# Kernel optimization log

Measured on AMD Instinct MI355X. Metric: run time of the kernel, lower is better.

Reference implementation:

```python
import jax, jax.numpy as jnp
import numpy as np

N_NODES = 100000
IN_DIM = 500
HID = 64
N_CLASSES = 47
N_EDGES = 1200000
K_LAYERS = 2


def _spmm_rownorm(edge_index, h, n):
    # Row-normalized D^{-1} A @ h via gather + segment_sum over edge list.
    src, dst = edge_index[0], edge_index[1]
    ones = jnp.ones(src.shape[0], dtype=h.dtype)
    deg = jax.ops.segment_sum(ones, src, num_segments=n)
    inv_deg = 1.0 / jnp.maximum(deg, 1.0)
    msg = h[dst] * inv_deg[src][:, None]  # [E, HID]
    return jax.ops.segment_sum(msg, src, num_segments=n)  # [N, HID]


def setup_inputs() -> dict:
    key = jax.random.key(0)
    ks = jax.random.split(key, 12)
    x = jax.random.normal(ks[0], (N_NODES, IN_DIM), dtype=jnp.float32)
    edge_index_1 = jax.random.randint(ks[1], (2, N_EDGES), 0, N_NODES, dtype=jnp.int32)
    edge_index_2 = jax.random.randint(ks[2], (2, N_EDGES), 0, N_NODES, dtype=jnp.int32)
    s = 0.02
    W_embed = jax.random.normal(ks[3], (IN_DIM, HID), dtype=jnp.float32) * s
    b_embed = jnp.zeros((HID,), dtype=jnp.float32)
    W0 = jax.random.normal(ks[4], (4 * HID, HID), dtype=jnp.float32) * s
    b0 = jnp.zeros((HID,), dtype=jnp.float32)
    W1 = jax.random.normal(ks[5], (4 * HID, HID), dtype=jnp.float32) * s
    b1 = jnp.zeros((HID,), dtype=jnp.float32)
    Wc = jax.random.normal(ks[6], (HID * (K_LAYERS + 1), N_CLASSES), dtype=jnp.float32) * s
    bc = jnp.zeros((N_CLASSES,), dtype=jnp.float32)
    return {"x": x, "edge_index_1": edge_index_1, "edge_index_2": edge_index_2,
            "W_embed": W_embed, "b_embed": b_embed, "W0": W0, "b0": b0,
            "W1": W1, "b1": b1, "Wc": Wc, "bc": bc}


def reference(x, edge_index_1, edge_index_2, W_embed, b_embed, W0, b0, W1, b1, Wc, bc):
    n = x.shape[0]
    r0 = jax.nn.relu(x @ W_embed + b_embed)  # dropout = identity in eval
    reps = [r0]
    r_prev = r0
    for (W, b) in ((W0, b0), (W1, b1)):
        n1 = _spmm_rownorm(edge_index_1, r_prev, n)
        n2 = _spmm_rownorm(edge_index_2, r_prev, n)
        concat = jnp.concatenate([r_prev, n1, r_prev, n2], axis=1)  # ego separation
        r_k = jax.nn.relu(concat @ W + b)
        reps.append(r_k)
        r_prev = r_k
    emb = jnp.concatenate(reps, axis=1)  # [N, HID*(K+1)]
    logits = emb @ Wc + bc
    return logits
```

## Files before the change

kernel.cpp:

```cpp
#include <hip/hip_runtime.h>

namespace {

constexpr int N  = 100000;
constexpr int KD = 500;
constexpr int E  = 1200000;
constexpr int NC = 47;

constexpr int M2  = 2 * N;
constexpr int E2  = 2 * E;
constexpr int NB  = 391;
constexpr int AB  = 586;
constexpr int EBMAX = 8192;

typedef __attribute__((ext_vector_type(8))) short short8;
typedef __attribute__((ext_vector_type(4))) float f32x4;

__device__ __forceinline__ ushort f2bf(float f) {
    union { float f; uint u; } c; c.f = f;
    uint u = c.u + 0x7fffu + ((c.u >> 16) & 1);
    return (ushort)(u >> 16);
}
__device__ __forceinline__ float bflo(uint v) { union { uint u; float f; } c; c.u = v << 16;        return c.f; }
__device__ __forceinline__ float bfhi(uint v) { union { uint u; float f; } c; c.u = v & 0xffff0000u; return c.f; }


__global__ __launch_bounds__(256) void prep_all(const float* __restrict__ We, const float* __restrict__ W0,
                                                const float* __restrict__ W1, const float* __restrict__ Wc,
                                                const float* __restrict__ bc,
                                                int* __restrict__ cursor, ushort* __restrict__ wtE,
                                                ushort* __restrict__ wf0, ushort* __restrict__ wf1,
                                                ushort* __restrict__ wct, float* __restrict__ bcp) {
    int i = blockIdx.x * 256 + threadIdx.x;
    if (i < NB) cursor[i] = i * EBMAX;
    if (i < 64 * 512) {
        int c = i >> 9, k = i & 511;
        wtE[i] = f2bf(k < KD ? We[k * 64 + c] : 0.f);
    }
    if (i < 64 * 192) {
        int c = i / 192, k = i % 192;
        float v0, v1;
        if (k < 64)       { v0 = W0[k * 64 + c] + W0[(128 + k) * 64 + c];
                            v1 = W1[k * 64 + c] + W1[(128 + k) * 64 + c]; }
        else if (k < 128) { v0 = W0[k * 64 + c]; v1 = W1[k * 64 + c]; }
        else              { v0 = W0[(k + 64) * 64 + c]; v1 = W1[(k + 64) * 64 + c]; }
        wf0[i] = f2bf(v0);
        wf1[i] = f2bf(v1);
        wct[i] = f2bf(c < NC ? Wc[k * NC + c] : 0.f);
    }
    if (i < 64) bcp[i] = (i < NC) ? bc[i] : 0.f;
}


__global__ __launch_bounds__(256) void bucket_scatter(const int* __restrict__ src1, const int* __restrict__ dst1,
                                                      const int* __restrict__ src2, const int* __restrict__ dst2,
                                                      int* __restrict__ cursor, uint* __restrict__ ebuf) {
    __shared__ int h[NB];
    __shared__ int claim[NB];
    int t = threadIdx.x;
    int mb[16];
    uint mu[16];
    for (int b = t; b < NB; b += 256) h[b] = 0;
    __syncthreads();
    #pragma unroll
    for (int q = 0; q < 16; ++q) {
        int i = blockIdx.x * 4096 + q * 256 + t;
        if (i < E2) {
            int g = i >= E;
            int idx = i - g * E;
            int s = g ? src2[idx] : src1[idx];
            int d = g ? dst2[idx] : dst1[idx];
            int v = g * N + s;
            mb[q] = v >> 9;
            mu[q] = ((uint)(v & 511) << 17) | (uint)d;
            atomicAdd(&h[mb[q]], 1);
        } else {
            mb[q] = -1;
            mu[q] = 0;
        }
    }
    __syncthreads();
    for (int b = t; b < NB; b += 256)
        claim[b] = h[b] ? atomicAdd(&cursor[b], h[b]) : 0;
    __syncthreads();
    for (int b = t; b < NB; b += 256) h[b] = 0;
    __syncthreads();
    #pragma unroll
    for (int q = 0; q < 16; ++q) {
        if (mb[q] >= 0) {
            int r = atomicAdd(&h[mb[q]], 1);
            ebuf[claim[mb[q]] + r] = mu[q];
        }
    }
}

__global__ __launch_bounds__(256) void csr_finalize(const uint* __restrict__ ebuf, const int* __restrict__ cursor,
                                                    int* __restrict__ rp, int* __restrict__ rpe,
                                                    float* __restrict__ invd, int* __restrict__ col) {
    __shared__ uint eb[EBMAX];
    __shared__ int h[512];
    __shared__ int ex[512];
    __shared__ int ps[256];
    int bid = blockIdx.x;
    int t = threadIdx.x;
    int b0 = bid * EBMAX;
    int cnt = cursor[bid] - b0;
    if (cnt > EBMAX) cnt = EBMAX;
    if (cnt < 0) cnt = 0;
    h[t] = 0; h[t + 256] = 0;
    for (int j = t; j < cnt; j += 256) eb[j] = ebuf[b0 + j];
    __syncthreads();
    for (int j = t; j < cnt; j += 256) atomicAdd(&h[eb[j] >> 17], 1);
    __syncthreads();
    int pv = h[2 * t] + h[2 * t + 1];
    ps[t] = pv;
    __syncthreads();
    for (int off = 1; off < 256; off <<= 1) {
        int x = (t >= off) ? ps[t - off] : 0;
        __syncthreads();
        ps[t] += x;
        __syncthreads();
    }
    int e2 = ps[t] - pv;
    ex[2 * t] = e2;
    ex[2 * t + 1] = e2 + h[2 * t];
    __syncthreads();
    #pragma unroll
    for (int q = 0; q < 2; ++q) {
        int k = q * 256 + t;
        int n = bid * 512 + k;
        if (n < M2) {
            int st = b0 + ex[k];
            int dv = h[k];
            rp[n]  = st;
            rpe[n] = st + dv;
            invd[n] = 1.0f / (float)(dv > 1 ? dv : 1);
        }
    }
    __syncthreads();
    for (int j = t; j < cnt; j += 256) {
        uint u = eb[j];
        int ls = u >> 17;
        int r = atomicAdd(&ex[ls], 1);
        col[b0 + r] = (int)(u & 0x1FFFFu) * 384;
    }
}


__device__ __forceinline__ void stageB(const ushort* __restrict__ Wt, int ldw, int k0, short* Bs) {
    const int tid = threadIdx.x;
    #pragma unroll
    for (int i = 0; i < 2; ++i) {
        int idx = tid + i * 256;
        int c = idx >> 3, qc = (idx & 7) * 8;
        uint4 v = *reinterpret_cast<const uint4*>(Wt + (size_t)c * ldw + k0 + qc);
        *reinterpret_cast<uint4*>(Bs + (((c << 6) + qc) ^ ((c & 7) << 3))) = v;
    }
}

__device__ __forceinline__ void mma64(const short* As, const short* Bs, f32x4 acc[2][4]) {
    const int lane = threadIdx.x & 63;
    const int wrow = (threadIdx.x >> 6) * 32;
    const int llo = lane & 15, lhi = lane >> 4;
    #pragma unroll
    for (int kf = 0; kf < 2; ++kf) {
        const int kb = kf * 32 + lhi * 8;
        short8 a[2], b[4];
        #pragma unroll
        for (int m = 0; m < 2; ++m) {
            int r = wrow + m * 16 + llo;
            a[m] = *reinterpret_cast<const short8*>(As + (((r << 6) + kb) ^ ((r & 7) << 3)));
        }
        #pragma unroll
        for (int n = 0; n < 4; ++n) {
            int c = n * 16 + llo;
            b[n] = *reinterpret_cast<const short8*>(Bs + (((c << 6) + kb) ^ ((c & 7) << 3)));
        }
        #pragma unroll
        for (int m = 0; m < 2; ++m)
            #pragma unroll
            for (int n = 0; n < 4; ++n)
                acc[m][n] = __builtin_amdgcn_mfma_f32_16x16x32_bf16(a[m], b[n], acc[m][n], 0, 0, 0);
    }
}

template<bool OUTF32>
__device__ __forceinline__ void epilogue(f32x4 acc[2][4], const float* __restrict__ bias,
                                         void* out, int ldo, int ocols, int relu, int rbase) {
    const int lane = threadIdx.x & 63;
    const int wrow = (threadIdx.x >> 6) * 32;
    #pragma unroll
    for (int m = 0; m < 2; ++m) {
        #pragma unroll
        for (int r = 0; r < 4; ++r) {
            int orow = rbase + wrow + m * 16 + (lane >> 4) * 4 + r;
            if (orow >= N) continue;
            #pragma unroll
            for (int n = 0; n < 4; ++n) {
                int c = n * 16 + (lane & 15);
                float v = acc[m][n][r] + bias[c];
                if (relu) v = fmaxf(v, 0.f);
                if (OUTF32) {
                    if (c < ocols) ((float*)out)[(size_t)orow * ldo + c] = v;
                } else {
                    ((ushort*)out)[(size_t)orow * ldo + c] = f2bf(v);
                }
            }
        }
    }
}

__global__ __launch_bounds__(256) void gemm_embed(const float* __restrict__ x,
                                                  const ushort* __restrict__ WtE,
                                                  const float* __restrict__ bias,
                                                  ushort* __restrict__ out) {
    __shared__ short As[128 * 64];
    __shared__ short Bs[64 * 64];
    const int tid = threadIdx.x;
    const int rbase = blockIdx.x * 128;
    f32x4 acc[2][4] = {};
    for (int k0 = 0; k0 < 512; k0 += 64) {
        __syncthreads();
        #pragma unroll
        for (int i = 0; i < 8; ++i) {
            int idx = tid + i * 256;
            int r = idx >> 4, qc = (idx & 15) * 4;
            int grow = rbase + r;
            float4 v = {0.f, 0.f, 0.f, 0.f};
            if (grow < N && k0 + qc < KD) v = *reinterpret_cast<const float4*>(x + (size_t)grow * KD + k0 + qc);
            uint2 p;
            p.x = (uint)f2bf(v.x) | ((uint)f2bf(v.y) << 16);
            p.y = (uint)f2bf(v.z) | ((uint)f2bf(v.w) << 16);
            *reinterpret_cast<uint2*>(As + (((r << 6) + qc) ^ ((r & 7) << 3))) = p;
        }
        stageB(WtE, 512, k0, Bs);
        __syncthreads();
        mma64(As, Bs, acc);
    }
    epilogue<false>(acc, bias, out, 192, 64, 1, rbase);
}

template<bool OUTF32>
__global__ __launch_bounds__(256) void gemm3(const ushort* __restrict__ a0, int lda0,
                                             const ushort* __restrict__ a1, int lda1,
                                             const ushort* __restrict__ a2, int lda2,
                                             const ushort* __restrict__ Wt,
                                             const float* __restrict__ bias,
                                             void* out, int ldo, int ocols, int relu) {
    __shared__ short As[128 * 64];
    __shared__ short Bs[64 * 64];
    const int tid = threadIdx.x;
    const int rbase = blockIdx.x * 128;
    f32x4 acc[2][4] = {};
    const ushort* aseg[3] = {a0, a1, a2};
    const int ldas[3] = {lda0, lda1, lda2};
    #pragma unroll
    for (int seg = 0; seg < 3; ++seg) {
        const ushort* A = aseg[seg];
        const int lda = ldas[seg];
        __syncthreads();
        #pragma unroll
        for (int i = 0; i < 4; ++i) {
            int idx = tid + i * 256;
            int r = idx >> 3, qc = (idx & 7) * 8;
            int grow = rbase + r;
            uint4 v = {0u, 0u, 0u, 0u};
            if (grow < N) v = *reinterpret_cast<const uint4*>(A + (size_t)grow * lda + qc);
            *reinterpret_cast<uint4*>(As + (((r << 6) + qc) ^ ((r & 7) << 3))) = v;
        }
        stageB(Wt, 192, seg * 64, Bs);
        __syncthreads();
        mma64(As, Bs, acc);
    }
    epilogue<OUTF32>(acc, bias, out, ldo, ocols, relu, rbase);
}


__global__ __launch_bounds__(256) void spmm7(const int* __restrict__ rp, const int* __restrict__ rpe,
                                             const int* __restrict__ col,
                                             const float* __restrict__ invd,
                                             const ushort* __restrict__ table, int colOff,
                                             ushort* __restrict__ n1b, ushort* __restrict__ n2b) {
    int gid = (blockIdx.x * 256 + threadIdx.x) >> 3;
    int ls = threadIdx.x & 7;
    if (gid >= M2) return;
    const char* hb = (const char*)(table + colOff) + ls * 16;
    float w = invd[gid];
    int s = rp[gid], e = rpe[gid];
    int e1 = e - 1;
    float a0=0.f,a1=0.f,a2=0.f,a3=0.f,a4=0.f,a5=0.f,a6=0.f,a7=0.f;
    for (int j = s; j < e; j += 8) {
        int off[8];
        float wv[8];
        #pragma unroll
        for (int u = 0; u < 8; ++u) {
            int jj = j + u;
            int cidx = jj < e ? jj : e1;
            off[u] = col[cidx];
            wv[u] = jj < e ? 1.f : 0.f;
        }
        uint4 v[8];
        #pragma unroll
        for (int u = 0; u < 8; ++u) v[u] = *reinterpret_cast<const uint4*>(hb + off[u]);
        #pragma unroll
        for (int u = 0; u < 8; ++u) {
            a0 = fmaf(wv[u], bflo(v[u].x), a0); a1 = fmaf(wv[u], bfhi(v[u].x), a1);
            a2 = fmaf(wv[u], bflo(v[u].y), a2); a3 = fmaf(wv[u], bfhi(v[u].y), a3);
            a4 = fmaf(wv[u], bflo(v[u].z), a4); a5 = fmaf(wv[u], bfhi(v[u].z), a5);
            a6 = fmaf(wv[u], bflo(v[u].w), a6); a7 = fmaf(wv[u], bfhi(v[u].w), a7);
        }
    }
    int g = gid >= N;
    int node = gid - g * N;
    ushort* op = g ? n2b : n1b;
    uint4 o;
    o.x = (uint)f2bf(a0 * w) | ((uint)f2bf(a1 * w) << 16);
    o.y = (uint)f2bf(a2 * w) | ((uint)f2bf(a3 * w) << 16);
    o.z = (uint)f2bf(a4 * w) | ((uint)f2bf(a5 * w) << 16);
    o.w = (uint)f2bf(a6 * w) | ((uint)f2bf(a7 * w) << 16);
    *reinterpret_cast<uint4*>(op + (size_t)node * 64 + ls * 8) = o;
}

}

extern "C" void kernel_launch(void* const* d_in, const int* in_sizes, int n_in,
                              void* d_out, int out_size, void* d_ws, size_t ws_size,
                              hipStream_t stream) {
    const float* x       = (const float*)d_in[0];
    const int*   ei1     = (const int*)d_in[1];
    const int*   ei2     = (const int*)d_in[2];
    const float* W_embed = (const float*)d_in[3];
    const float* b_embed = (const float*)d_in[4];
    const float* W0      = (const float*)d_in[5];
    const float* b0      = (const float*)d_in[6];
    const float* W1      = (const float*)d_in[7];
    const float* b1      = (const float*)d_in[8];
    const float* Wc      = (const float*)d_in[9];
    const float* bc      = (const float*)d_in[10];
    float* out = (float*)d_out;

    char* ws = (char*)d_ws;
    size_t off = 0;
    auto alloc = [&](size_t bytes) -> void* {
        void* p = ws + off;
        off += (bytes + 255) & ~(size_t)255;
        return p;
    };

    ushort* embB  = (ushort*)alloc((size_t)N * 192 * 2);
    ushort* n1b   = (ushort*)alloc((size_t)N * 64 * 2);
    ushort* n2b   = (ushort*)alloc((size_t)N * 64 * 2);
    int*    col   = (int*)alloc((size_t)NB * EBMAX * 4);
    uint*   ebuf  = (uint*)alloc((size_t)NB * EBMAX * 4);
    int*    rp    = (int*)alloc((size_t)M2 * 4);
    int*    rpe   = (int*)alloc((size_t)M2 * 4);
    float*  invd  = (float*)alloc((size_t)M2 * 4);
    int*    bcur  = (int*)alloc((NB + 1) * 4);
    ushort* wtE   = (ushort*)alloc(64 * 512 * 2);
    ushort* weff0 = (ushort*)alloc(64 * 192 * 2);
    ushort* weff1 = (ushort*)alloc(64 * 192 * 2);
    ushort* wct   = (ushort*)alloc(64 * 192 * 2);
    float*  bcp   = (float*)alloc(64 * 4);
    if (off > ws_size) return;

    const int* src1 = ei1, *dst1 = ei1 + E;
    const int* src2 = ei2, *dst2 = ei2 + E;

    const int GB = (N + 127) / 128;
    const int PB = (M2 * 8 + 255) / 256;

    prep_all<<<128, 256, 0, stream>>>(W_embed, W0, W1, Wc, bc, bcur, wtE, weff0, weff1, wct, bcp);

    bucket_scatter<<<AB, 256, 0, stream>>>(src1, dst1, src2, dst2, bcur, ebuf);
    csr_finalize<<<NB, 256, 0, stream>>>(ebuf, bcur, rp, rpe, invd, col);

    gemm_embed<<<GB, 256, 0, stream>>>(x, wtE, b_embed, embB);

    for (int layer = 0; layer < 2; ++layer) {
        const ushort* rprev = embB + 64 * layer;
        spmm7<<<PB, 256, 0, stream>>>(rp, rpe, col, invd, embB, 64 * layer, n1b, n2b);
        const ushort* Wl = (layer == 0) ? weff0 : weff1;
        const float*  bl = (layer == 0) ? b0 : b1;
        gemm3<false><<<GB, 256, 0, stream>>>(rprev, 192, n1b, 64, n2b, 64, Wl, bl,
                                             embB + 64 * (layer + 1), 192, 64, 1);
    }

    gemm3<true><<<GB, 256, 0, stream>>>(embB, 192, embB + 64, 192, embB + 128, 192, wct, bcp,
                                        out, NC, NC, 0);
}
```

Measured before the change: 231.0 us.

## Merge CSR finalize with embed GEMM and degree-sort SpMM node schedule

The CSR finalize and the embedding GEMM become one launch that shares memory through a union, so the two independent stages can run at the same time on different CUs. The finalize blocks also counting-sort the nodes of each 512-node bucket by degree and write a permutation. spmm7 walks that permutation so the 8-lane groups in a wavefront handle nodes of similar degree, which cuts divergence from uneven loop trip counts. The costs are an extra indirection load per node, scattered output writes, and the larger shared-memory footprint of the merged kernel, which may lower occupancy for the GEMM blocks.

```diff
diff --git a/kernel.cpp b/kernel.cpp
--- a/kernel.cpp
+++ b/kernel.cpp
@@ -10,6 +10,7 @@
 constexpr int M2  = 2 * N;
 constexpr int E2  = 2 * E;
 constexpr int NB  = 391;
+constexpr int MP  = NB * 512;
 constexpr int AB  = 586;
 constexpr int EBMAX = 8192;
 
@@ -94,58 +95,6 @@
     }
 }
 
-__global__ __launch_bounds__(256) void csr_finalize(const uint* __restrict__ ebuf, const int* __restrict__ cursor,
-                                                    int* __restrict__ rp, int* __restrict__ rpe,
-                                                    float* __restrict__ invd, int* __restrict__ col) {
-    __shared__ uint eb[EBMAX];
-    __shared__ int h[512];
-    __shared__ int ex[512];
-    __shared__ int ps[256];
-    int bid = blockIdx.x;
-    int t = threadIdx.x;
-    int b0 = bid * EBMAX;
-    int cnt = cursor[bid] - b0;
-    if (cnt > EBMAX) cnt = EBMAX;
-    if (cnt < 0) cnt = 0;
-    h[t] = 0; h[t + 256] = 0;
-    for (int j = t; j < cnt; j += 256) eb[j] = ebuf[b0 + j];
-    __syncthreads();
-    for (int j = t; j < cnt; j += 256) atomicAdd(&h[eb[j] >> 17], 1);
-    __syncthreads();
-    int pv = h[2 * t] + h[2 * t + 1];
-    ps[t] = pv;
-    __syncthreads();
-    for (int off = 1; off < 256; off <<= 1) {
-        int x = (t >= off) ? ps[t - off] : 0;
-        __syncthreads();
-        ps[t] += x;
-        __syncthreads();
-    }
-    int e2 = ps[t] - pv;
-    ex[2 * t] = e2;
-    ex[2 * t + 1] = e2 + h[2 * t];
-    __syncthreads();
-    #pragma unroll
-    for (int q = 0; q < 2; ++q) {
-        int k = q * 256 + t;
-        int n = bid * 512 + k;
-        if (n < M2) {
-            int st = b0 + ex[k];
-            int dv = h[k];
-            rp[n]  = st;
-            rpe[n] = st + dv;
-            invd[n] = 1.0f / (float)(dv > 1 ? dv : 1);
-        }
-    }
-    __syncthreads();
-    for (int j = t; j < cnt; j += 256) {
-        uint u = eb[j];
-        int ls = u >> 17;
-        int r = atomicAdd(&ex[ls], 1);
-        col[b0 + r] = (int)(u & 0x1FFFFu) * 384;
-    }
-}
-
 
 __device__ __forceinline__ void stageB(const ushort* __restrict__ Wt, int ldw, int k0, short* Bs) {
     const int tid = threadIdx.x;
@@ -210,34 +159,118 @@
     }
 }
 
-__global__ __launch_bounds__(256) void gemm_embed(const float* __restrict__ x,
-                                                  const ushort* __restrict__ WtE,
-                                                  const float* __restrict__ bias,
-                                                  ushort* __restrict__ out) {
-    __shared__ short As[128 * 64];
-    __shared__ short Bs[64 * 64];
-    const int tid = threadIdx.x;
-    const int rbase = blockIdx.x * 128;
-    f32x4 acc[2][4] = {};
-    for (int k0 = 0; k0 < 512; k0 += 64) {
-        __syncthreads();
-        #pragma unroll
-        for (int i = 0; i < 8; ++i) {
-            int idx = tid + i * 256;
-            int r = idx >> 4, qc = (idx & 15) * 4;
-            int grow = rbase + r;
-            float4 v = {0.f, 0.f, 0.f, 0.f};
-            if (grow < N && k0 + qc < KD) v = *reinterpret_cast<const float4*>(x + (size_t)grow * KD + k0 + qc);
-            uint2 p;
-            p.x = (uint)f2bf(v.x) | ((uint)f2bf(v.y) << 16);
-            p.y = (uint)f2bf(v.z) | ((uint)f2bf(v.w) << 16);
-            *reinterpret_cast<uint2*>(As + (((r << 6) + qc) ^ ((r & 7) << 3))) = p;
-        }
-        stageB(WtE, 512, k0, Bs);
-        __syncthreads();
-        mma64(As, Bs, acc);
-    }
-    epilogue<false>(acc, bias, out, 192, 64, 1, rbase);
+
+union SMem {
+    struct { uint eb[EBMAX]; int h[512]; int ex[512]; int ps[256]; } f;
+    struct { short As[128 * 64]; short Bs[64 * 64]; } g;
+};
+
+__global__ __launch_bounds__(256) void embed_finalize(
+        const float* __restrict__ x, const ushort* __restrict__ WtE,
+        const float* __restrict__ bias, ushort* __restrict__ out,
+        const uint* __restrict__ ebuf, const int* __restrict__ cursor,
+        int* __restrict__ rp, int* __restrict__ rpe, float* __restrict__ invd,
+        int* __restrict__ col, int* __restrict__ nodePerm) {
+    __shared__ SMem sm;
+    const int t = threadIdx.x;
+    if (blockIdx.x < NB) {
+        int bid = blockIdx.x;
+        int b0 = bid * EBMAX;
+        int cnt = cursor[bid] - b0;
+        if (cnt > EBMAX) cnt = EBMAX;
+        if (cnt < 0) cnt = 0;
+        sm.f.h[t] = 0; sm.f.h[t + 256] = 0;
+        for (int j = t; j < cnt; j += 256) sm.f.eb[j] = ebuf[b0 + j];
+        __syncthreads();
+        for (int j = t; j < cnt; j += 256) atomicAdd(&sm.f.h[sm.f.eb[j] >> 17], 1);
+        __syncthreads();
+        int pv = sm.f.h[2 * t] + sm.f.h[2 * t + 1];
+        sm.f.ps[t] = pv;
+        __syncthreads();
+        for (int off = 1; off < 256; off <<= 1) {
+            int xv = (t >= off) ? sm.f.ps[t - off] : 0;
+            __syncthreads();
+            sm.f.ps[t] += xv;
+            __syncthreads();
+        }
+        int e2 = sm.f.ps[t] - pv;
+        sm.f.ex[2 * t] = e2;
+        sm.f.ex[2 * t + 1] = e2 + sm.f.h[2 * t];
+        __syncthreads();
+        #pragma unroll
+        for (int q = 0; q < 2; ++q) {
+            int k = q * 256 + t;
+            int n = bid * 512 + k;
+            if (n < M2) {
+                int st = b0 + sm.f.ex[k];
+                int dv = sm.f.h[k];
+                rp[n]  = st;
+                rpe[n] = st + dv;
+                invd[n] = 1.0f / (float)(dv > 1 ? dv : 1);
+            }
+        }
+        __syncthreads();
+        for (int j = t; j < cnt; j += 256) {
+            uint u = sm.f.eb[j];
+            int ls = u >> 17;
+            int r = atomicAdd(&sm.f.ex[ls], 1);
+            col[b0 + r] = (int)(u & 0x1FFFFu) * 384;
+        }
+        __syncthreads();
+        int* dh  = (int*)sm.f.eb;
+        int* dex = ((int*)sm.f.eb) + 512;
+        dh[t] = 0; dh[t + 256] = 0;
+        __syncthreads();
+        #pragma unroll
+        for (int q = 0; q < 2; ++q) {
+            int k = q * 256 + t;
+            int d = sm.f.h[k]; if (d > 511) d = 511;
+            atomicAdd(&dh[d], 1);
+        }
+        __syncthreads();
+        int pv2 = dh[2 * t] + dh[2 * t + 1];
+        sm.f.ps[t] = pv2;
+        __syncthreads();
+        for (int off = 1; off < 256; off <<= 1) {
+            int xv = (t >= off) ? sm.f.ps[t - off] : 0;
+            __syncthreads();
+            sm.f.ps[t] += xv;
+            __syncthreads();
+        }
+        int e3 = sm.f.ps[t] - pv2;
+        dex[2 * t] = e3;
+        dex[2 * t + 1] = e3 + dh[2 * t];
+        __syncthreads();
+        #pragma unroll
+        for (int q = 0; q < 2; ++q) {
+            int k = q * 256 + t;
+            int d = sm.f.h[k]; if (d > 511) d = 511;
+            int pos = atomicAdd(&dex[d], 1);
+            nodePerm[bid * 512 + pos] = bid * 512 + k;
+        }
+    } else {
+        const int rbase = (blockIdx.x - NB) * 128;
+        f32x4 acc[2][4] = {};
+        for (int k0 = 0; k0 < 512; k0 += 64) {
+            __syncthreads();
+            #pragma unroll
+            for (int i = 0; i < 8; ++i) {
+                int idx = t + i * 256;
+                int r = idx >> 4, qc = (idx & 15) * 4;
+                int grow = rbase + r;
+                float4 v = {0.f, 0.f, 0.f, 0.f};
+                if (grow < N && k0 + qc < KD) v = *reinterpret_cast<const float4*>(x + (size_t)grow * KD + k0 + qc);
+                uint2 p;
+                p.x = (uint)f2bf(v.x) | ((uint)f2bf(v.y) << 16);
+                p.y = (uint)f2bf(v.z) | ((uint)f2bf(v.w) << 16);
+                *reinterpret_cast<uint2*>(sm.g.As + (((r << 6) + qc) ^ ((r & 7) << 3))) = p;
+            }
+            stageB(WtE, 512, k0, sm.g.Bs);
+            __syncthreads();
+            mma64(sm.g.As, sm.g.Bs, acc);
+        }
+        epilogue<false>(acc, bias, out, 192, 64, 1, rbase);
+    }
 }
 
 template<bool OUTF32>
@@ -279,14 +312,17 @@
 __global__ __launch_bounds__(256) void spmm7(const int* __restrict__ rp, const int* __restrict__ rpe,
                                              const int* __restrict__ col,
                                              const float* __restrict__ invd,
+                                             const int* __restrict__ nodePerm,
                                              const ushort* __restrict__ table, int colOff,
                                              ushort* __restrict__ n1b, ushort* __restrict__ n2b) {
-    int gid = (blockIdx.x * 256 + threadIdx.x) >> 3;
+    int sched = (blockIdx.x * 256 + threadIdx.x) >> 3;
     int ls = threadIdx.x & 7;
-    if (gid >= M2) return;
+    if (sched >= MP) return;
+    int node = nodePerm[sched];
+    if (node >= M2) return;
     const char* hb = (const char*)(table + colOff) + ls * 16;
-    float w = invd[gid];
-    int s = rp[gid], e = rpe[gid];
+    float w = invd[node];
+    int s = rp[node], e = rpe[node];
     int e1 = e - 1;
     float a0=0.f,a1=0.f,a2=0.f,a3=0.f,a4=0.f,a5=0.f,a6=0.f,a7=0.f;
     for (int j = s; j < e; j += 8) {
@@ -310,15 +346,15 @@
             a6 = fmaf(wv[u], bflo(v[u].w), a6); a7 = fmaf(wv[u], bfhi(v[u].w), a7);
         }
     }
-    int g = gid >= N;
-    int node = gid - g * N;
+    int g = node >= N;
+    int onode = node - g * N;
     ushort* op = g ? n2b : n1b;
     uint4 o;
     o.x = (uint)f2bf(a0 * w) | ((uint)f2bf(a1 * w) << 16);
     o.y = (uint)f2bf(a2 * w) | ((uint)f2bf(a3 * w) << 16);
     o.z = (uint)f2bf(a4 * w) | ((uint)f2bf(a5 * w) << 16);
     o.w = (uint)f2bf(a6 * w) | ((uint)f2bf(a7 * w) << 16);
-    *reinterpret_cast<uint4*>(op + (size_t)node * 64 + ls * 8) = o;
+    *reinterpret_cast<uint4*>(op + (size_t)onode * 64 + ls * 8) = o;
 }
 
 }
@@ -355,6 +391,7 @@
     int*    rp    = (int*)alloc((size_t)M2 * 4);
     int*    rpe   = (int*)alloc((size_t)M2 * 4);
     float*  invd  = (float*)alloc((size_t)M2 * 4);
+    int*    nperm = (int*)alloc((size_t)MP * 4);
     int*    bcur  = (int*)alloc((NB + 1) * 4);
     ushort* wtE   = (ushort*)alloc(64 * 512 * 2);
     ushort* weff0 = (ushort*)alloc(64 * 192 * 2);
@@ -367,18 +404,18 @@
     const int* src2 = ei2, *dst2 = ei2 + E;
 
     const int GB = (N + 127) / 128;
-    const int PB = (M2 * 8 + 255) / 256;
+    const int PB = (MP * 8 + 255) / 256;
 
     prep_all<<<128, 256, 0, stream>>>(W_embed, W0, W1, Wc, bc, bcur, wtE, weff0, weff1, wct, bcp);
 
     bucket_scatter<<<AB, 256, 0, stream>>>(src1, dst1, src2, dst2, bcur, ebuf);
-    csr_finalize<<<NB, 256, 0, stream>>>(ebuf, bcur, rp, rpe, invd, col);
-
-    gemm_embed<<<GB, 256, 0, stream>>>(x, wtE, b_embed, embB);
+
+    embed_finalize<<<NB + GB, 256, 0, stream>>>(x, wtE, b_embed, embB,
+                                                ebuf, bcur, rp, rpe, invd, col, nperm);
 
     for (int layer = 0; layer < 2; ++layer) {
         const ushort* rprev = embB + 64 * layer;
-        spmm7<<<PB, 256, 0, stream>>>(rp, rpe, col, invd, embB, 64 * layer, n1b, n2b);
+        spmm7<<<PB, 256, 0, stream>>>(rp, rpe, col, invd, nperm, embB, 64 * layer, n1b, n2b);
         const ushort* Wl = (layer == 0) ? weff0 : weff1;
         const float*  bl = (layer == 0) ? b0 : b1;
         gemm3<false><<<GB, 256, 0, stream>>>(rprev, 192, n1b, 64, n2b, 64, Wl, bl,
```

After: 255.1 us. 1.1x slower.

## Schedule SpMM rows sorted by degree within each bucket to reduce wave divergence

Applied to the files above, without the earlier changes.

csr_finalize now runs a second counting sort that orders the 512 rows of each bucket by degree and writes a node permutation. spmm7 reads that permutation, so the 8 row-groups in a wavefront have similar edge counts and the loop trip count varies less across lanes. The cost is an extra indirection load per row group, more work in csr_finalize, and output writes that are no longer contiguous. Nodes in the padding range (beyond 2N) exit early.

```diff
diff --git a/kernel.cpp b/kernel.cpp
--- a/kernel.cpp
+++ b/kernel.cpp
@@ -10,6 +10,7 @@
 constexpr int M2  = 2 * N;
 constexpr int E2  = 2 * E;
 constexpr int NB  = 391;
+constexpr int MP  = NB * 512;
 constexpr int AB  = 586;
 constexpr int EBMAX = 8192;
 
@@ -96,7 +97,8 @@
 
 __global__ __launch_bounds__(256) void csr_finalize(const uint* __restrict__ ebuf, const int* __restrict__ cursor,
                                                     int* __restrict__ rp, int* __restrict__ rpe,
-                                                    float* __restrict__ invd, int* __restrict__ col) {
+                                                    float* __restrict__ invd, int* __restrict__ col,
+                                                    int* __restrict__ nodePerm) {
     __shared__ uint eb[EBMAX];
     __shared__ int h[512];
     __shared__ int ex[512];
@@ -116,9 +118,9 @@
     ps[t] = pv;
     __syncthreads();
     for (int off = 1; off < 256; off <<= 1) {
-        int x = (t >= off) ? ps[t - off] : 0;
-        __syncthreads();
-        ps[t] += x;
+        int xv = (t >= off) ? ps[t - off] : 0;
+        __syncthreads();
+        ps[t] += xv;
         __syncthreads();
     }
     int e2 = ps[t] - pv;
@@ -143,6 +145,38 @@
         int ls = u >> 17;
         int r = atomicAdd(&ex[ls], 1);
         col[b0 + r] = (int)(u & 0x1FFFFu) * 384;
+    }
+    __syncthreads();
+    int* dh  = (int*)eb;
+    int* dex = ((int*)eb) + 512;
+    dh[t] = 0; dh[t + 256] = 0;
+    __syncthreads();
+    #pragma unroll
+    for (int q = 0; q < 2; ++q) {
+        int k = q * 256 + t;
+        int d = h[k]; if (d > 511) d = 511;
+        atomicAdd(&dh[d], 1);
+    }
+    __syncthreads();
+    int pv2 = dh[2 * t] + dh[2 * t + 1];
+    ps[t] = pv2;
+    __syncthreads();
+    for (int off = 1; off < 256; off <<= 1) {
+        int xv = (t >= off) ? ps[t - off] : 0;
+        __syncthreads();
+        ps[t] += xv;
+        __syncthreads();
+    }
+    int e3 = ps[t] - pv2;
+    dex[2 * t] = e3;
+    dex[2 * t + 1] = e3 + dh[2 * t];
+    __syncthreads();
+    #pragma unroll
+    for (int q = 0; q < 2; ++q) {
+        int k = q * 256 + t;
+        int d = h[k]; if (d > 511) d = 511;
+        int pos = atomicAdd(&dex[d], 1);
+        nodePerm[bid * 512 + pos] = bid * 512 + k;
     }
 }
 
@@ -279,14 +313,17 @@
 __global__ __launch_bounds__(256) void spmm7(const int* __restrict__ rp, const int* __restrict__ rpe,
                                              const int* __restrict__ col,
                                              const float* __restrict__ invd,
+                                             const int* __restrict__ nodePerm,
                                              const ushort* __restrict__ table, int colOff,
                                              ushort* __restrict__ n1b, ushort* __restrict__ n2b) {
-    int gid = (blockIdx.x * 256 + threadIdx.x) >> 3;
+    int sched = (blockIdx.x * 256 + threadIdx.x) >> 3;
     int ls = threadIdx.x & 7;
-    if (gid >= M2) return;
+    if (sched >= MP) return;
+    int node = nodePerm[sched];
+    if (node >= M2) return;
     const char* hb = (const char*)(table + colOff) + ls * 16;
-    float w = invd[gid];
-    int s = rp[gid], e = rpe[gid];
+    float w = invd[node];
+    int s = rp[node], e = rpe[node];
     int e1 = e - 1;
     float a0=0.f,a1=0.f,a2=0.f,a3=0.f,a4=0.f,a5=0.f,a6=0.f,a7=0.f;
     for (int j = s; j < e; j += 8) {
@@ -310,15 +347,15 @@
             a6 = fmaf(wv[u], bflo(v[u].w), a6); a7 = fmaf(wv[u], bfhi(v[u].w), a7);
         }
     }
-    int g = gid >= N;
-    int node = gid - g * N;
+    int g = node >= N;
+    int onode = node - g * N;
     ushort* op = g ? n2b : n1b;
     uint4 o;
     o.x = (uint)f2bf(a0 * w) | ((uint)f2bf(a1 * w) << 16);
     o.y = (uint)f2bf(a2 * w) | ((uint)f2bf(a3 * w) << 16);
     o.z = (uint)f2bf(a4 * w) | ((uint)f2bf(a5 * w) << 16);
     o.w = (uint)f2bf(a6 * w) | ((uint)f2bf(a7 * w) << 16);
-    *reinterpret_cast<uint4*>(op + (size_t)node * 64 + ls * 8) = o;
+    *reinterpret_cast<uint4*>(op + (size_t)onode * 64 + ls * 8) = o;
 }
 
 }
@@ -355,6 +392,7 @@
     int*    rp    = (int*)alloc((size_t)M2 * 4);
     int*    rpe   = (int*)alloc((size_t)M2 * 4);
     float*  invd  = (float*)alloc((size_t)M2 * 4);
+    int*    nperm = (int*)alloc((size_t)MP * 4);
     int*    bcur  = (int*)alloc((NB + 1) * 4);
     ushort* wtE   = (ushort*)alloc(64 * 512 * 2);
     ushort* weff0 = (ushort*)alloc(64 * 192 * 2);
@@ -367,18 +405,18 @@
     const int* src2 = ei2, *dst2 = ei2 + E;
 
     const int GB = (N + 127) / 128;
-    const int PB = (M2 * 8 + 255) / 256;
+    const int PB = (MP * 8 + 255) / 256;
 
     prep_all<<<128, 256, 0, stream>>>(W_embed, W0, W1, Wc, bc, bcur, wtE, weff0, weff1, wct, bcp);
 
     bucket_scatter<<<AB, 256, 0, stream>>>(src1, dst1, src2, dst2, bcur, ebuf);
-    csr_finalize<<<NB, 256, 0, stream>>>(ebuf, bcur, rp, rpe, invd, col);
+    csr_finalize<<<NB, 256, 0, stream>>>(ebuf, bcur, rp, rpe, invd, col, nperm);
 
     gemm_embed<<<GB, 256, 0, stream>>>(x, wtE, b_embed, embB);
 
     for (int layer = 0; layer < 2; ++layer) {
         const ushort* rprev = embB + 64 * layer;
-        spmm7<<<PB, 256, 0, stream>>>(rp, rpe, col, invd, embB, 64 * layer, n1b, n2b);
+        spmm7<<<PB, 256, 0, stream>>>(rp, rpe, col, invd, nperm, embB, 64 * layer, n1b, n2b);
         const ushort* Wl = (layer == 0) ? weff0 : weff1;
         const float*  bl = (layer == 0) ? b0 : b1;
         gemm3<false><<<GB, 256, 0, stream>>>(rprev, 192, n1b, 64, n2b, 64, Wl, bl,
```

New measurement: 256.5 us. 1.11x slower.

## Fuse SpMM aggregation into layer GEMM and merge edge scatter with embed GEMM

Applied to the files above, without the earlier changes.

The sparse neighbor aggregation is now computed inside the per-layer GEMM kernel, written straight into the shared-memory A tile instead of round-tripping n1/n2 through global memory. The edge bucket scatter and the embedding GEMM run in one launch with disjoint block ranges, so the two independent jobs can overlap and a launch is dropped. The trade-off is that the gather runs with only GB blocks of 256 threads, each doing 4 rows per thread-group serially, which may reduce memory-level parallelism compared with the standalone SpMM grid.

```diff
diff --git a/kernel.cpp b/kernel.cpp
--- a/kernel.cpp
+++ b/kernel.cpp
@@ -52,45 +52,140 @@
 }
 
 
-__global__ __launch_bounds__(256) void bucket_scatter(const int* __restrict__ src1, const int* __restrict__ dst1,
-                                                      const int* __restrict__ src2, const int* __restrict__ dst2,
-                                                      int* __restrict__ cursor, uint* __restrict__ ebuf) {
-    __shared__ int h[NB];
-    __shared__ int claim[NB];
-    int t = threadIdx.x;
-    int mb[16];
-    uint mu[16];
-    for (int b = t; b < NB; b += 256) h[b] = 0;
-    __syncthreads();
-    #pragma unroll
-    for (int q = 0; q < 16; ++q) {
-        int i = blockIdx.x * 4096 + q * 256 + t;
-        if (i < E2) {
-            int g = i >= E;
-            int idx = i - g * E;
-            int s = g ? src2[idx] : src1[idx];
-            int d = g ? dst2[idx] : dst1[idx];
-            int v = g * N + s;
-            mb[q] = v >> 9;
-            mu[q] = ((uint)(v & 511) << 17) | (uint)d;
-            atomicAdd(&h[mb[q]], 1);
-        } else {
-            mb[q] = -1;
-            mu[q] = 0;
-        }
-    }
-    __syncthreads();
-    for (int b = t; b < NB; b += 256)
-        claim[b] = h[b] ? atomicAdd(&cursor[b], h[b]) : 0;
-    __syncthreads();
-    for (int b = t; b < NB; b += 256) h[b] = 0;
-    __syncthreads();
-    #pragma unroll
-    for (int q = 0; q < 16; ++q) {
-        if (mb[q] >= 0) {
-            int r = atomicAdd(&h[mb[q]], 1);
-            ebuf[claim[mb[q]] + r] = mu[q];
-        }
+__device__ __forceinline__ void stageB(const ushort* __restrict__ Wt, int ldw, int k0, short* Bs) {
+    const int tid = threadIdx.x;
+    #pragma unroll
+    for (int i = 0; i < 2; ++i) {
+        int idx = tid + i * 256;
+        int c = idx >> 3, qc = (idx & 7) * 8;
+        uint4 v = *reinterpret_cast<const uint4*>(Wt + (size_t)c * ldw + k0 + qc);
+        *reinterpret_cast<uint4*>(Bs + (((c << 6) + qc) ^ ((c & 7) << 3))) = v;
+    }
+}
+
+__device__ __forceinline__ void mma64(const short* As, const short* Bs, f32x4 acc[2][4]) {
+    const int lane = threadIdx.x & 63;
+    const int wrow = (threadIdx.x >> 6) * 32;
+    const int llo = lane & 15, lhi = lane >> 4;
+    #pragma unroll
+    for (int kf = 0; kf < 2; ++kf) {
+        const int kb = kf * 32 + lhi * 8;
+        short8 a[2], b[4];
+        #pragma unroll
+        for (int m = 0; m < 2; ++m) {
+            int r = wrow + m * 16 + llo;
+            a[m] = *reinterpret_cast<const short8*>(As + (((r << 6) + kb) ^ ((r & 7) << 3)));
+        }
+        #pragma unroll
+        for (int n = 0; n < 4; ++n) {
+            int c = n * 16 + llo;
+            b[n] = *reinterpret_cast<const short8*>(Bs + (((c << 6) + kb) ^ ((c & 7) << 3)));
+        }
+        #pragma unroll
+        for (int m = 0; m < 2; ++m)
+            #pragma unroll
+            for (int n = 0; n < 4; ++n)
+                acc[m][n] = __builtin_amdgcn_mfma_f32_16x16x32_bf16(a[m], b[n], acc[m][n], 0, 0, 0);
+    }
+}
+
+template<bool OUTF32>
+__device__ __forceinline__ void epilogue(f32x4 acc[2][4], const float* __restrict__ bias,
+                                         void* out, int ldo, int ocols, int relu, int rbase) {
+    const int lane = threadIdx.x & 63;
+    const int wrow = (threadIdx.x >> 6) * 32;
+    #pragma unroll
+    for (int m = 0; m < 2; ++m) {
+        #pragma unroll
+        for (int r = 0; r < 4; ++r) {
+            int orow = rbase + wrow + m * 16 + (lane >> 4) * 4 + r;
+            if (orow >= N) continue;
+            #pragma unroll
+            for (int n = 0; n < 4; ++n) {
+                int c = n * 16 + (lane & 15);
+                float v = acc[m][n][r] + bias[c];
+                if (relu) v = fmaxf(v, 0.f);
+                if (OUTF32) {
+                    if (c < ocols) ((float*)out)[(size_t)orow * ldo + c] = v;
+                } else {
+                    ((ushort*)out)[(size_t)orow * ldo + c] = f2bf(v);
+                }
+            }
+        }
+    }
+}
+
+
+union SMem2 {
+    struct { int h[NB]; int claim[NB]; } s;
+    struct { short As[128 * 64]; short Bs[64 * 64]; } g;
+};
+
+__global__ __launch_bounds__(256) void scatter_embed(
+        const int* __restrict__ src1, const int* __restrict__ dst1,
+        const int* __restrict__ src2, const int* __restrict__ dst2,
+        int* __restrict__ cursor, uint* __restrict__ ebuf,
+        const float* __restrict__ x, const ushort* __restrict__ WtE,
+        const float* __restrict__ bias, ushort* __restrict__ out) {
+    __shared__ SMem2 sm;
+    const int t = threadIdx.x;
+    if (blockIdx.x < AB) {
+        int mb[16];
+        uint mu[16];
+        for (int b = t; b < NB; b += 256) sm.s.h[b] = 0;
+        __syncthreads();
+        #pragma unroll
+        for (int q = 0; q < 16; ++q) {
+            int i = blockIdx.x * 4096 + q * 256 + t;
+            if (i < E2) {
+                int g = i >= E;
+                int idx = i - g * E;
+                int s = g ? src2[idx] : src1[idx];
+                int d = g ? dst2[idx] : dst1[idx];
+                int v = g * N + s;
+                mb[q] = v >> 9;
+                mu[q] = ((uint)(v & 511) << 17) | (uint)d;
+                atomicAdd(&sm.s.h[mb[q]], 1);
+            } else {
+                mb[q] = -1;
+                mu[q] = 0;
+            }
+        }
+        __syncthreads();
+        for (int b = t; b < NB; b += 256)
+            sm.s.claim[b] = sm.s.h[b] ? atomicAdd(&cursor[b], sm.s.h[b]) : 0;
+        __syncthreads();
+        for (int b = t; b < NB; b += 256) sm.s.h[b] = 0;
+        __syncthreads();
+        #pragma unroll
+        for (int q = 0; q < 16; ++q) {
+            if (mb[q] >= 0) {
+                int r = atomicAdd(&sm.s.h[mb[q]], 1);
+                ebuf[sm.s.claim[mb[q]] + r] = mu[q];
+            }
+        }
+    } else {
+        const int rbase = (blockIdx.x - AB) * 128;
+        f32x4 acc[2][4] = {};
+        for (int k0 = 0; k0 < 512; k0 += 64) {
+            __syncthreads();
+            #pragma unroll
+            for (int i = 0; i < 8; ++i) {
+                int idx = t + i * 256;
+                int r = idx >> 4, qc = (idx & 15) * 4;
+                int grow = rbase + r;
+                float4 v = {0.f, 0.f, 0.f, 0.f};
+                if (grow < N && k0 + qc < KD) v = *reinterpret_cast<const float4*>(x + (size_t)grow * KD + k0 + qc);
+                uint2 p;
+                p.x = (uint)f2bf(v.x) | ((uint)f2bf(v.y) << 16);
+                p.y = (uint)f2bf(v.z) | ((uint)f2bf(v.w) << 16);
+                *reinterpret_cast<uint2*>(sm.g.As + (((r << 6) + qc) ^ ((r & 7) << 3))) = p;
+            }
+            stageB(WtE, 512, k0, sm.g.Bs);
+            __syncthreads();
+            mma64(sm.g.As, sm.g.Bs, acc);
+        }
+        epilogue<false>(acc, bias, out, 192, 64, 1, rbase);
     }
 }
 
@@ -116,9 +211,9 @@
     ps[t] = pv;
     __syncthreads();
     for (int off = 1; off < 256; off <<= 1) {
-        int x = (t >= off) ? ps[t - off] : 0;
-        __syncthreads();
-        ps[t] += x;
+        int xv = (t >= off) ? ps[t - off] : 0;
+        __syncthreads();
+        ps[t] += xv;
         __syncthreads();
     }
     int e2 = ps[t] - pv;
@@ -147,71 +242,11 @@
 }
 
 
-__device__ __forceinline__ void stageB(const ushort* __restrict__ Wt, int ldw, int k0, short* Bs) {
-    const int tid = threadIdx.x;
-    #pragma unroll
-    for (int i = 0; i < 2; ++i) {
-        int idx = tid + i * 256;
-        int c = idx >> 3, qc = (idx & 7) * 8;
-        uint4 v = *reinterpret_cast<const uint4*>(Wt + (size_t)c * ldw + k0 + qc);
-        *reinterpret_cast<uint4*>(Bs + (((c << 6) + qc) ^ ((c & 7) << 3))) = v;
-    }
-}
-
-__device__ __forceinline__ void mma64(const short* As, const short* Bs, f32x4 acc[2][4]) {
-    const int lane = threadIdx.x & 63;
-    const int wrow = (threadIdx.x >> 6) * 32;
-    const int llo = lane & 15, lhi = lane >> 4;
-    #pragma unroll
-    for (int kf = 0; kf < 2; ++kf) {
-        const int kb = kf * 32 + lhi * 8;
-        short8 a[2], b[4];
-        #pragma unroll
-        for (int m = 0; m < 2; ++m) {
-            int r = wrow + m * 16 + llo;
-            a[m] = *reinterpret_cast<const short8*>(As + (((r << 6) + kb) ^ ((r & 7) << 3)));
-        }
-        #pragma unroll
-        for (int n = 0; n < 4; ++n) {
-            int c = n * 16 + llo;
-            b[n] = *reinterpret_cast<const short8*>(Bs + (((c << 6) + kb) ^ ((c & 7) << 3)));
-        }
-        #pragma unroll
-        for (int m = 0; m < 2; ++m)
-            #pragma unroll
-            for (int n = 0; n < 4; ++n)
-                acc[m][n] = __builtin_amdgcn_mfma_f32_16x16x32_bf16(a[m], b[n], acc[m][n], 0, 0, 0);
-    }
-}
-
-template<bool OUTF32>
-__device__ __forceinline__ void epilogue(f32x4 acc[2][4], const float* __restrict__ bias,
-                                         void* out, int ldo, int ocols, int relu, int rbase) {
-    const int lane = threadIdx.x & 63;
-    const int wrow = (threadIdx.x >> 6) * 32;
-    #pragma unroll
-    for (int m = 0; m < 2; ++m) {
-        #pragma unroll
-        for (int r = 0; r < 4; ++r) {
-            int orow = rbase + wrow + m * 16 + (lane >> 4) * 4 + r;
-            if (orow >= N) continue;
-            #pragma unroll
-            for (int n = 0; n < 4; ++n) {
-                int c = n * 16 + (lane & 15);
-                float v = acc[m][n][r] + bias[c];
-                if (relu) v = fmaxf(v, 0.f);
-                if (OUTF32) {
-                    if (c < ocols) ((float*)out)[(size_t)orow * ldo + c] = v;
-                } else {
-                    ((ushort*)out)[(size_t)orow * ldo + c] = f2bf(v);
-                }
-            }
-        }
-    }
-}
-
-__global__ __launch_bounds__(256) void gemm_embed(const float* __restrict__ x,
-                                                  const ushort* __restrict__ WtE,
+__global__ __launch_bounds__(256) void gemm_layer(const ushort* __restrict__ rprev,
+                                                  const ushort* __restrict__ table, int colOff,
+                                                  const int* __restrict__ rp, const int* __restrict__ rpe,
+                                                  const int* __restrict__ col, const float* __restrict__ invd,
+                                                  const ushort* __restrict__ Wt,
                                                   const float* __restrict__ bias,
                                                   ushort* __restrict__ out) {
     __shared__ short As[128 * 64];
@@ -219,45 +254,88 @@
     const int tid = threadIdx.x;
     const int rbase = blockIdx.x * 128;
     f32x4 acc[2][4] = {};
-    for (int k0 = 0; k0 < 512; k0 += 64) {
-        __syncthreads();
-        #pragma unroll
-        for (int i = 0; i < 8; ++i) {
-            int idx = tid + i * 256;
-            int r = idx >> 4, qc = (idx & 15) * 4;
+
+    #pragma unroll
+    for (int i = 0; i < 4; ++i) {
+        int idx = tid + i * 256;
+        int r = idx >> 3, qc = (idx & 7) * 8;
+        int grow = rbase + r;
+        uint4 v = {0u, 0u, 0u, 0u};
+        if (grow < N) v = *reinterpret_cast<const uint4*>(rprev + (size_t)grow * 192 + qc);
+        *reinterpret_cast<uint4*>(As + (((r << 6) + qc) ^ ((r & 7) << 3))) = v;
+    }
+    stageB(Wt, 192, 0, Bs);
+    __syncthreads();
+    mma64(As, Bs, acc);
+
+    const int row = tid >> 3;
+    const int ls  = tid & 7;
+    const char* hb = (const char*)(table + colOff) + ls * 16;
+    #pragma unroll
+    for (int g = 0; g < 2; ++g) {
+        __syncthreads();
+        #pragma unroll
+        for (int sw = 0; sw < 4; ++sw) {
+            int r = sw * 32 + row;
             int grow = rbase + r;
-            float4 v = {0.f, 0.f, 0.f, 0.f};
-            if (grow < N && k0 + qc < KD) v = *reinterpret_cast<const float4*>(x + (size_t)grow * KD + k0 + qc);
-            uint2 p;
-            p.x = (uint)f2bf(v.x) | ((uint)f2bf(v.y) << 16);
-            p.y = (uint)f2bf(v.z) | ((uint)f2bf(v.w) << 16);
-            *reinterpret_cast<uint2*>(As + (((r << 6) + qc) ^ ((r & 7) << 3))) = p;
-        }
-        stageB(WtE, 512, k0, Bs);
+            uint4 o = {0u, 0u, 0u, 0u};
+            if (grow < N) {
+                int node = grow + g * N;
+                float w = invd[node];
+                int s = rp[node], e = rpe[node];
+                int e1 = e - 1;
+                float a0=0.f,a1=0.f,a2=0.f,a3=0.f,a4=0.f,a5=0.f,a6=0.f,a7=0.f;
+                for (int j = s; j < e; j += 8) {
+                    int off[8];
+                    float wv[8];
+                    #pragma unroll
+                    for (int u = 0; u < 8; ++u) {
+                        int jj = j + u;
+                        int cidx = jj < e ? jj : e1;
+                        off[u] = col[cidx];
+                        wv[u] = jj < e ? 1.f : 0.f;
+                    }
+                    uint4 v[8];
+                    #pragma unroll
+                    for (int u = 0; u < 8; ++u) v[u] = *reinterpret_cast<const uint4*>(hb + off[u]);
+                    #pragma unroll
+                    for (int u = 0; u < 8; ++u) {
+                        a0 = fmaf(wv[u], bflo(v[u].x), a0); a1 = fmaf(wv[u], bfhi(v[u].x), a1);
+                        a2 = fmaf(wv[u], bflo(v[u].y), a2); a3 = fmaf(wv[u], bfhi(v[u].y), a3);
+                        a4 = fmaf(wv[u], bflo(v[u].z), a4); a5 = fmaf(wv[u], bfhi(v[u].z), a5);
+                        a6 = fmaf(wv[u], bflo(v[u].w), a6); a7 = fmaf(wv[u], bfhi(v[u].w), a7);
+                    }
+                }
+                o.x = (uint)f2bf(a0 * w) | ((uint)f2bf(a1 * w) << 16);
+                o.y = (uint)f2bf(a2 * w) | ((uint)f2bf(a3 * w) << 16);
+                o.z = (uint)f2bf(a4 * w) | ((uint)f2bf(a5 * w) << 16);
+                o.w = (uint)f2bf(a6 * w) | ((uint)f2bf(a7 * w) << 16);
+            }
+            *reinterpret_cast<uint4*>(As + (((r << 6) + ls * 8) ^ ((r & 7) << 3))) = o;
+        }
+        stageB(Wt, 192, (1 + g) * 64, Bs);
         __syncthreads();
         mma64(As, Bs, acc);
     }
     epilogue<false>(acc, bias, out, 192, 64, 1, rbase);
 }
 
-template<bool OUTF32>
-__global__ __launch_bounds__(256) void gemm3(const ushort* __restrict__ a0, int lda0,
-                                             const ushort* __restrict__ a1, int lda1,
-                                             const ushort* __restrict__ a2, int lda2,
-                                             const ushort* __restrict__ Wt,
-                                             const float* __restrict__ bias,
-                                             void* out, int ldo, int ocols, int relu) {
+
+__global__ __launch_bounds__(256) void gemm_cls(const ushort* __restrict__ a0,
+                                                const ushort* __restrict__ a1,
+                                                const ushort* __restrict__ a2,
+                                                const ushort* __restrict__ Wt,
+                                                const float* __restrict__ bias,
+                                                float* __restrict__ out) {
     __shared__ short As[128 * 64];
     __shared__ short Bs[64 * 64];
     const int tid = threadIdx.x;
     const int rbase = blockIdx.x * 128;
     f32x4 acc[2][4] = {};
     const ushort* aseg[3] = {a0, a1, a2};
-    const int ldas[3] = {lda0, lda1, lda2};
     #pragma unroll
     for (int seg = 0; seg < 3; ++seg) {
         const ushort* A = aseg[seg];
-        const int lda = ldas[seg];
         __syncthreads();
         #pragma unroll
         for (int i = 0; i < 4; ++i) {
@@ -265,60 +343,14 @@
             int r = idx >> 3, qc = (idx & 7) * 8;
             int grow = rbase + r;
             uint4 v = {0u, 0u, 0u, 0u};
-            if (grow < N) v = *reinterpret_cast<const uint4*>(A + (size_t)grow * lda + qc);
+            if (grow < N) v = *reinterpret_cast<const uint4*>(A + (size_t)grow * 192 + qc);
             *reinterpret_cast<uint4*>(As + (((r << 6) + qc) ^ ((r & 7) << 3))) = v;
         }
         stageB(Wt, 192, seg * 64, Bs);
         __syncthreads();
         mma64(As, Bs, acc);
     }
-    epilogue<OUTF32>(acc, bias, out, ldo, ocols, relu, rbase);
-}
-
-
-__global__ __launch_bounds__(256) void spmm7(const int* __restrict__ rp, const int* __restrict__ rpe,
-                                             const int* __restrict__ col,
-                                             const float* __restrict__ invd,
-                                             const ushort* __restrict__ table, int colOff,
-                                             ushort* __restrict__ n1b, ushort* __restrict__ n2b) {
-    int gid = (blockIdx.x * 256 + threadIdx.x) >> 3;
-    int ls = threadIdx.x & 7;
-    if (gid >= M2) return;
-    const char* hb = (const char*)(table + colOff) + ls * 16;
-    float w = invd[gid];
-    int s = rp[gid], e = rpe[gid];
-    int e1 = e - 1;
-    float a0=0.f,a1=0.f,a2=0.f,a3=0.f,a4=0.f,a5=0.f,a6=0.f,a7=0.f;
-    for (int j = s; j < e; j += 8) {
-        int off[8];
-        float wv[8];
-        #pragma unroll
-        for (int u = 0; u < 8; ++u) {
-            int jj = j + u;
-            int cidx = jj < e ? jj : e1;
-            off[u] = col[cidx];
-            wv[u] = jj < e ? 1.f : 0.f;
-        }
-        uint4 v[8];
-        #pragma unroll
-        for (int u = 0; u < 8; ++u) v[u] = *reinterpret_cast<const uint4*>(hb + off[u]);
-        #pragma unroll
-        for (int u = 0; u < 8; ++u) {
-            a0 = fmaf(wv[u], bflo(v[u].x), a0); a1 = fmaf(wv[u], bfhi(v[u].x), a1);
-            a2 = fmaf(wv[u], bflo(v[u].y), a2); a3 = fmaf(wv[u], bfhi(v[u].y), a3);
-            a4 = fmaf(wv[u], bflo(v[u].z), a4); a5 = fmaf(wv[u], bfhi(v[u].z), a5);
-            a6 = fmaf(wv[u], bflo(v[u].w), a6); a7 = fmaf(wv[u], bfhi(v[u].w), a7);
-        }
-    }
-    int g = gid >= N;
-    int node = gid - g * N;
-    ushort* op = g ? n2b : n1b;
-    uint4 o;
-    o.x = (uint)f2bf(a0 * w) | ((uint)f2bf(a1 * w) << 16);
-    o.y = (uint)f2bf(a2 * w) | ((uint)f2bf(a3 * w) << 16);
-    o.z = (uint)f2bf(a4 * w) | ((uint)f2bf(a5 * w) << 16);
-    o.w = (uint)f2bf(a6 * w) | ((uint)f2bf(a7 * w) << 16);
-    *reinterpret_cast<uint4*>(op + (size_t)node * 64 + ls * 8) = o;
+    epilogue<true>(acc, bias, out, NC, NC, 0, rbase);
 }
 
 }
@@ -348,8 +380,6 @@
     };
 
     ushort* embB  = (ushort*)alloc((size_t)N * 192 * 2);
-    ushort* n1b   = (ushort*)alloc((size_t)N * 64 * 2);
-    ushort* n2b   = (ushort*)alloc((size_t)N * 64 * 2);
     int*    col   = (int*)alloc((size_t)NB * EBMAX * 4);
     uint*   ebuf  = (uint*)alloc((size_t)NB * EBMAX * 4);
     int*    rp    = (int*)alloc((size_t)M2 * 4);
@@ -367,24 +397,21 @@
     const int* src2 = ei2, *dst2 = ei2 + E;
 
     const int GB = (N + 127) / 128;
-    const int PB = (M2 * 8 + 255) / 256;
 
     prep_all<<<128, 256, 0, stream>>>(W_embed, W0, W1, Wc, bc, bcur, wtE, weff0, weff1, wct, bcp);
 
-    bucket_scatter<<<AB, 256, 0, stream>>>(src1, dst1, src2, dst2, bcur, ebuf);
+    scatter_embed<<<AB + GB, 256, 0, stream>>>(src1, dst1, src2, dst2, bcur, ebuf,
+                                               x, wtE, b_embed, embB);
+
     csr_finalize<<<NB, 256, 0, stream>>>(ebuf, bcur, rp, rpe, invd, col);
-
-    gemm_embed<<<GB, 256, 0, stream>>>(x, wtE, b_embed, embB);
 
     for (int layer = 0; layer < 2; ++layer) {
         const ushort* rprev = embB + 64 * layer;
-        spmm7<<<PB, 256, 0, stream>>>(rp, rpe, col, invd, embB, 64 * layer, n1b, n2b);
         const ushort* Wl = (layer == 0) ? weff0 : weff1;
         const float*  bl = (layer == 0) ? b0 : b1;
-        gemm3<false><<<GB, 256, 0, stream>>>(rprev, 192, n1b, 64, n2b, 64, Wl, bl,
-                                             embB + 64 * (layer + 1), 192, 64, 1);
-    }
-
-    gemm3<true><<<GB, 256, 0, stream>>>(embB, 192, embB + 64, 192, embB + 128, 192, wct, bcp,
-                                        out, NC, NC, 0);
-}
+        gemm_layer<<<GB, 256, 0, stream>>>(rprev, embB, 64 * layer, rp, rpe, col, invd,
+                                           Wl, bl, embB + 64 * (layer + 1));
+    }
+
+    gemm_cls<<<GB, 256, 0, stream>>>(embB, embB + 64, embB + 128, wct, bcp, out);
+}
```

Measured after the change: 306.9 us. 32.9% more time.
